# Kernel tuning notes

Hardware: AMD Instinct MI355X
Metric: run time of the kernel (lower is better)

The kernel has to match this reference:

```python
import jax, jax.numpy as jnp
import numpy as np


def _lstm_scan(x_seq, W, U, b):
    # x_seq: [T, in_dim]; Keras gate order i, f, g(c), o; sigmoid/tanh activations.
    units = W.shape[1] // 4
    xz = x_seq @ W + b  # [T, 4*units], precompute input contribution

    def step(carry, xz_t):
        h, c = carry
        z = xz_t + h @ U
        i, f, g, o = jnp.split(z, 4)
        i = jax.nn.sigmoid(i)
        f = jax.nn.sigmoid(f)
        g = jnp.tanh(g)
        o = jax.nn.sigmoid(o)
        c_new = f * c + i * g
        h_new = o * jnp.tanh(c_new)
        return (h_new, c_new), h_new

    h0 = jnp.zeros((units,), dtype=x_seq.dtype)
    c0 = jnp.zeros((units,), dtype=x_seq.dtype)
    (_, _), hs = jax.lax.scan(step, (h0, c0), xz)
    return hs  # [T, units]


def setup_inputs() -> dict:
    key = jax.random.key(0)
    ks = jax.random.split(key, 6)
    var_num, g_dim, d, vocab = 256, 1024, 512, 32000
    s = lambda fi, fo: (2.0 / (fi + fo)) ** 0.5
    return {
        "context": jax.random.normal(ks[0], (var_num, g_dim), jnp.float32),
        "Wm": jax.random.normal(ks[1], (g_dim, d), jnp.float32) * s(g_dim, d),
        "bm": jnp.zeros((d,), jnp.float32),
        "W": jax.random.normal(ks[2], (d, 4 * d), jnp.float32) * s(d, 4 * d),
        "U": jax.random.normal(ks[3], (d, 4 * d), jnp.float32) * s(d, 4 * d),
        "b": jnp.zeros((4 * d,), jnp.float32),
        "Wl": jax.random.normal(ks[4], (d, vocab), jnp.float32) * s(d, vocab),
        "bl": jnp.zeros((vocab,), jnp.float32),
        "max_subtoken_len": 8,
    }


def reference(context, Wm, bm, W, U, b, Wl, bl, max_subtoken_len):
    # Dense merge of func/graph embedding (cat_func_g_emb branch)
    merged = context @ Wm + bm  # [var_num, d]
    var_num = merged.shape[0]
    # Original loop feeds the SAME [1, var_num, d] sequence through the LSTM
    # max_subtoken_len times, carrying (h, c) across iterations => one long
    # scan over the tiled sequence of length S * var_num.
    x_seq = jnp.tile(merged, (max_subtoken_len, 1))  # [S*var_num, d]
    hs = _lstm_scan(x_seq, W, U, b)  # [S*var_num, units]
    hs = hs.reshape(max_subtoken_len, var_num, -1)  # [S, var_num, units]
    logits = jnp.einsum("svd,dk->svk", hs, Wl) + bl  # [S, var_num, vocab]
    return jnp.transpose(logits, (1, 0, 2))  # [var_num, S, vocab]
```

## Files before the change

kernel.cpp:

```cpp
#include <hip/hip_runtime.h>
#include <stdint.h>

#define D 512
#define T 2048
#define VOCAB 32000
#define NWG 16

typedef __attribute__((ext_vector_type(8))) short short8;
typedef __attribute__((ext_vector_type(4))) float f32x4;
typedef __attribute__((ext_vector_type(8))) unsigned short u16x8;
typedef __attribute__((ext_vector_type(2))) __fp16 f16x2;

__device__ __forceinline__ float fast_rcp(float x) { return __builtin_amdgcn_rcpf(x); }
__device__ __forceinline__ float sigm(float x) { return fast_rcp(1.0f + __expf(-x)); }
__device__ __forceinline__ float tanh_fast(float x) {
  float e = __expf(2.0f * x);
  return 1.0f - 2.0f * fast_rcp(e + 1.0f);
}
__device__ __forceinline__ unsigned short f2bf(float f) {
  unsigned u = __float_as_uint(f);
  unsigned r = u + 0x7fffu + ((u >> 16) & 1u);
  return (unsigned short)(r >> 16);
}
__device__ __forceinline__ uint64_t AL(const uint64_t* p) {
  return __hip_atomic_load(p, __ATOMIC_RELAXED, __HIP_MEMORY_SCOPE_AGENT);
}
union U32H2 { unsigned u; f16x2 h; };

__global__ __launch_bounds__(512) void prep_kernel(
    const float* __restrict__ ctx, const float* __restrict__ Wm,
    const float* __restrict__ bm, const float* __restrict__ W,
    const float* __restrict__ b, float* __restrict__ xz)
{
  __shared__ float ctx_s[4][1024];
  __shared__ float mg_s[4][512];
  const int tid = threadIdx.x;
  const int r0 = blockIdx.x * 4;

  for (int i = tid; i < 1024; i += 512) {
    int rr = i >> 8, c4 = (i & 255) * 4;
    *(float4*)&ctx_s[rr][c4] = *(const float4*)&ctx[(size_t)(r0 + rr) * 1024 + c4];
  }
  __syncthreads();
  {
    const int rr = tid >> 7, cg = (tid & 127) * 4;
    float a0 = bm[cg], a1 = bm[cg + 1], a2 = bm[cg + 2], a3 = bm[cg + 3];
    for (int k = 0; k < 1024; k += 4) {
      float4 cv = *(float4*)&ctx_s[rr][k];
      #pragma unroll
      for (int kk = 0; kk < 4; kk++) {
        float cc = (kk == 0) ? cv.x : (kk == 1) ? cv.y : (kk == 2) ? cv.z : cv.w;
        float4 wv = *(const float4*)&Wm[(size_t)(k + kk) * 512 + cg];
        a0 += cc * wv.x; a1 += cc * wv.y; a2 += cc * wv.z; a3 += cc * wv.w;
      }
    }
    *(float4*)&mg_s[rr][cg] = make_float4(a0, a1, a2, a3);
  }
  __syncthreads();
  {
    const int rr = tid >> 7, cg = (tid & 127) * 16;
    float acc[16];
    #pragma unroll
    for (int c = 0; c < 16; c++) acc[c] = b[cg + c];
    for (int k = 0; k < 512; k += 4) {
      float4 mv = *(float4*)&mg_s[rr][k];
      #pragma unroll
      for (int kk = 0; kk < 4; kk++) {
        float cc = (kk == 0) ? mv.x : (kk == 1) ? mv.y : (kk == 2) ? mv.z : mv.w;
        #pragma unroll
        for (int c4 = 0; c4 < 4; c4++) {
          float4 wv = *(const float4*)&W[(size_t)(k + kk) * 2048 + cg + c4 * 4];
          acc[c4 * 4 + 0] += cc * wv.x; acc[c4 * 4 + 1] += cc * wv.y;
          acc[c4 * 4 + 2] += cc * wv.z; acc[c4 * 4 + 3] += cc * wv.w;
        }
      }
    }
    #pragma unroll
    for (int c4 = 0; c4 < 4; c4++)
      *(float4*)&xz[(size_t)(r0 + rr) * 2048 + cg + c4 * 4] =
          make_float4(acc[c4 * 4], acc[c4 * 4 + 1], acc[c4 * 4 + 2], acc[c4 * 4 + 3]);
  }
}

__global__ __launch_bounds__(256) void wl_convert_kernel(
    const float* __restrict__ Wl, unsigned short* __restrict__ Wlt)
{
  const int c = blockIdx.x * 256 + threadIdx.x;
  for (int k8 = 0; k8 < 64; k8++) {
    u16x8 v;
    #pragma unroll
    for (int e = 0; e < 8; e++)
      v[e] = f2bf(Wl[(size_t)(k8 * 8 + e) * VOCAB + c]);
    *(u16x8*)&Wlt[(size_t)c * 512 + k8 * 8] = v;
  }
}

__global__ __launch_bounds__(256) void uconv2_kernel(
    const float* __restrict__ U, unsigned* __restrict__ Upr)
{
  const int blk = blockIdx.x;
  const int wg = blk >> 4, cb = blk & 15;
  const int rb = threadIdx.x & 31, ep = threadIdx.x >> 5;
  const int u0 = wg * 32 + cb * 2;
  const int r = rb + 64 * ep;
  unsigned outv[8];
  #pragma unroll
  for (int g = 0; g < 4; g++) {
    float2 lo = *(const float2*)&U[(size_t)r * 2048 + g * 512 + u0];
    float2 hi = *(const float2*)&U[(size_t)(r + 32) * 2048 + g * 512 + u0];
    U32H2 w0; w0.h[0] = (__fp16)lo.x; w0.h[1] = (__fp16)hi.x;
    U32H2 w1; w1.h[0] = (__fp16)lo.y; w1.h[1] = (__fp16)hi.y;
    outv[g * 2] = w0.u; outv[g * 2 + 1] = w1.u;
  }
  unsigned* dst = Upr + ((size_t)(wg * 512 + cb * 32 + rb)) * 64 + ep * 8;
  *(uint4*)dst = make_uint4(outv[0], outv[1], outv[2], outv[3]);
  *(uint4*)(dst + 4) = make_uint4(outv[4], outv[5], outv[6], outv[7]);
}

__global__
__attribute__((amdgpu_flat_work_group_size(512, 512)))
__attribute__((amdgpu_waves_per_eu(2, 2)))
void lstm_kernel(
    const float* __restrict__ xz, const unsigned* __restrict__ Upr,
    uint64_t* __restrict__ hb, unsigned short* __restrict__ hs)
{
  __shared__ float h_lds[2][512];
  const int tid = threadIdx.x;
  const int wg = blockIdx.x;
  const int rb = tid & 31;
  const int lane = tid & 63;
  const int cb = tid >> 5;
  const int u0 = wg * 32 + cb * 2;
  const bool gl = (rb < 2);
  const bool mypoll = (tid < 128) && ((tid >> 3) != wg);

  const unsigned* ubase = Upr + ((size_t)(wg * 512 + tid)) * 64;
  uint4 uv[16];
  #pragma unroll
  for (int i = 0; i < 16; i++) {
    const unsigned* ap = ubase + i * 4;
    asm volatile("global_load_dwordx4 %0, %1, off" : "=v"(uv[i]) : "v"(ap));
  }
  asm volatile("s_waitcnt vmcnt(0)" ::: "memory");
  unsigned u2[8][8];
  #pragma unroll
  for (int ep = 0; ep < 8; ep++) {
    uint4 a = uv[ep * 2], b4 = uv[ep * 2 + 1];
    u2[ep][0] = a.x; u2[ep][1] = a.y; u2[ep][2] = a.z; u2[ep][3] = a.w;
    u2[ep][4] = b4.x; u2[ep][5] = b4.y; u2[ep][6] = b4.z; u2[ep][7] = b4.w;
  }

  h_lds[0][tid] = 0.0f;
  float creg = 0.0f;
  const int b0 = rb & 1, b1 = (rb >> 1) & 1, b2v = (rb >> 2) & 1;

  for (int t = 0; t < T; t++) {
    #pragma unroll
    for (int ep = 0; ep < 8; ep++) {
      #pragma unroll
      for (int c = 0; c < 8; c++) asm volatile("" : "+v"(u2[ep][c]));
    }
    float xv0, xv1, xv2, xv3;
    if (gl) {
      const float* xp = &xz[(size_t)(t & 255) * 2048 + u0 + rb];
      xv0 = xp[0]; xv1 = xp[512]; xv2 = xp[1024]; xv3 = xp[1536];
    }
    const int par = t & 1;
    if (mypoll) {
      uint64_t* hw = hb + ((size_t)par << 9) + tid * 4;
      const unsigned tt = (unsigned)t;
      for (;;) {
        uint64_t w0 = AL(hw), w1 = AL(hw + 1), w2 = AL(hw + 2), w3 = AL(hw + 3);
        if (((unsigned)(w0 >> 32) == tt) & ((unsigned)(w1 >> 32) == tt) &
            ((unsigned)(w2 >> 32) == tt) & ((unsigned)(w3 >> 32) == tt)) {
          h_lds[par][tid * 4 + 0] = __uint_as_float((unsigned)w0);
          h_lds[par][tid * 4 + 1] = __uint_as_float((unsigned)w1);
          h_lds[par][tid * 4 + 2] = __uint_as_float((unsigned)w2);
          h_lds[par][tid * 4 + 3] = __uint_as_float((unsigned)w3);
          break;
        }
      }
    }
    __syncthreads();

    float zp[8];
    #pragma unroll
    for (int c = 0; c < 8; c++) zp[c] = 0.0f;
    #pragma unroll
    for (int ep = 0; ep < 8; ep++) {
      float hlo = h_lds[par][rb + 64 * ep];
      float hhi = h_lds[par][rb + 64 * ep + 32];
      f16x2 h2 = __builtin_amdgcn_cvt_pkrtz(hlo, hhi);
      #pragma unroll
      for (int c = 0; c < 8; c++) {
        U32H2 w; w.u = u2[ep][c];
        zp[c] = __builtin_amdgcn_fdot2(h2, w.h, zp[c], false);
      }
    }
    float q[4];
    #pragma unroll
    for (int j = 0; j < 4; j++) {
      float send = b0 ? zp[2 * j] : zp[2 * j + 1];
      float recv = __shfl_xor(send, 1, 64);
      q[j] = (b0 ? zp[2 * j + 1] : zp[2 * j]) + recv;
    }
    float r2[2];
    #pragma unroll
    for (int j = 0; j < 2; j++) {
      float send = b1 ? q[2 * j] : q[2 * j + 1];
      float recv = __shfl_xor(send, 2, 64);
      r2[j] = (b1 ? q[2 * j + 1] : q[2 * j]) + recv;
    }
    float z;
    {
      float send = b2v ? r2[0] : r2[1];
      float recv = __shfl_xor(send, 4, 64);
      z = (b2v ? r2[1] : r2[0]) + recv;
    }
    z += __shfl_xor(z, 8, 64);
    z += __shfl_xor(z, 16, 64);
    float zf = __shfl(z, (lane & 32) + 2 + b0, 64);
    float zg = __shfl(z, (lane & 32) + 4 + b0, 64);
    float zo = __shfl(z, (lane & 32) + 6 + b0, 64);

    if (gl) {
      float ig = sigm(z + xv0);
      float fg = sigm(zf + xv1);
      float gg = tanh_fast(zg + xv2);
      float og = sigm(zo + xv3);
      creg = fg * creg + ig * gg;
      float h = og * tanh_fast(creg);
      uint64_t pk = ((uint64_t)(unsigned)(t + 1) << 32) | (uint64_t)__float_as_uint(h);
      __hip_atomic_store(&hb[((size_t)((t + 1) & 1) << 9) + u0 + rb], pk,
                         __ATOMIC_RELAXED, __HIP_MEMORY_SCOPE_AGENT);
      h_lds[(t + 1) & 1][u0 + rb] = h;
      hs[(size_t)t * 512 + u0 + rb] = f2bf(h);
    }
  }
}

__global__ __launch_bounds__(512) void logits_kernel(
    const unsigned short* __restrict__ hs, const unsigned short* __restrict__ Wlt,
    const float* __restrict__ bl, float* __restrict__ out)
{
  __shared__ unsigned short As[128][40];
  __shared__ unsigned short Bs[256][40];
  const int tid = threadIdx.x;
  const int bx = blockIdx.x, by = blockIdx.y;
  const int lane = tid & 63, w = tid >> 6;
  const int wr = w >> 2, wc = w & 3;

  f32x4 acc[4][4];
  #pragma unroll
  for (int i = 0; i < 4; i++) {
    #pragma unroll
    for (int j = 0; j < 4; j++) acc[i][j] = (f32x4){0.0f, 0.0f, 0.0f, 0.0f};
  }

  for (int kk = 0; kk < 512; kk += 32) {
    {
      int r = tid >> 2, c8 = (tid & 3) * 8;
      *(uint4*)&As[r][c8] = *(const uint4*)&hs[(size_t)(by * 128 + r) * 512 + kk + c8];
    }
    #pragma unroll
    for (int i = 0; i < 2; i++) {
      int chunk = tid * 2 + i;
      int r = chunk >> 2, c8 = (chunk & 3) * 8;
      *(uint4*)&Bs[r][c8] = *(const uint4*)&Wlt[(size_t)(bx * 256 + r) * 512 + kk + c8];
    }
    __syncthreads();
    short8 af[4], bf[4];
    #pragma unroll
    for (int fr = 0; fr < 4; fr++)
      af[fr] = *(const short8*)&As[wr * 64 + fr * 16 + (lane & 15)][(lane >> 4) * 8];
    #pragma unroll
    for (int fc = 0; fc < 4; fc++)
      bf[fc] = *(const short8*)&Bs[wc * 64 + fc * 16 + (lane & 15)][(lane >> 4) * 8];
    #pragma unroll
    for (int fr = 0; fr < 4; fr++) {
      #pragma unroll
      for (int fc = 0; fc < 4; fc++)
        acc[fr][fc] = __builtin_amdgcn_mfma_f32_16x16x32_bf16(af[fr], bf[fc], acc[fr][fc], 0, 0, 0);
    }
    __syncthreads();
  }

  #pragma unroll
  for (int fc = 0; fc < 4; fc++) {
    int col = bx * 256 + wc * 64 + fc * 16 + (lane & 15);
    float blv = bl[col];
    #pragma unroll
    for (int fr = 0; fr < 4; fr++) {
      int row0 = by * 128 + wr * 64 + fr * 16 + (lane >> 4) * 4;
      #pragma unroll
      for (int j = 0; j < 4; j++) {
        int row = row0 + j;
        int orow = (row & 255) * 8 + (row >> 8);
        out[(size_t)orow * VOCAB + col] = acc[fr][fc][j] + blv;
      }
    }
  }
}

extern "C" void kernel_launch(void* const* d_in, const int* in_sizes, int n_in,
                              void* d_out, int out_size, void* d_ws, size_t ws_size,
                              hipStream_t stream)
{
  const float* ctx = (const float*)d_in[0];
  const float* Wm  = (const float*)d_in[1];
  const float* bm  = (const float*)d_in[2];
  const float* W   = (const float*)d_in[3];
  const float* U   = (const float*)d_in[4];
  const float* b   = (const float*)d_in[5];
  const float* Wl  = (const float*)d_in[6];
  const float* bl  = (const float*)d_in[7];
  float* out = (float*)d_out;

  char* ws = (char*)d_ws;
  uint64_t* hb        = (uint64_t*)ws;
  float* xz           = (float*)(ws + 65536);
  unsigned short* hs  = (unsigned short*)(ws + 65536 + (1 << 21));
  unsigned* Upr       = (unsigned*)(ws + 65536 + (2 << 21));
  unsigned short* Wlt = (unsigned short*)(ws + 65536 + (3 << 21));

  hipMemsetAsync(hb, 0, 8192, stream);
  prep_kernel<<<dim3(64), dim3(512), 0, stream>>>(ctx, Wm, bm, W, b, xz);
  uconv2_kernel<<<dim3(256), dim3(256), 0, stream>>>(U, Upr);
  wl_convert_kernel<<<dim3(125), dim3(256), 0, stream>>>(Wl, Wlt);

  void* args[] = { (void*)&xz, (void*)&Upr, (void*)&hb, (void*)&hs };
  hipLaunchCooperativeKernel((void*)lstm_kernel, dim3(NWG), dim3(512), args, 0, stream);

  logits_kernel<<<dim3(125, 16), dim3(512), 0, stream>>>(hs, Wlt, bl, out);
}
```

Measured before the change: 4.759 ms.

## Split LSTM workgroup into compute and polling waves with 256-thread reduction

The recurrent kernel now gives the first 256 threads the matvec, with each thread holding twice as many fp16 U weights in registers and reducing over 16 lanes instead of 32. The other 256 threads only poll the global h buffer for the next step and write it into LDS. The next step's xz values are prefetched right after the gate math, so their latency overlaps the poll. This aims to shorten the shuffle reduction and hide synchronization latency, at the cost of more registers per compute thread and a slower U repacking kernel launched with only 16 blocks.

Measured after the change: 4.834 ms. Within noise of the previous version (+1.6%).

```diff
diff --git a/kernel.cpp b/kernel.cpp
--- a/kernel.cpp
+++ b/kernel.cpp
@@ -95,26 +95,28 @@
   }
 }
 
-__global__ __launch_bounds__(256) void uconv2_kernel(
+__global__ __launch_bounds__(256) void uconv3_kernel(
     const float* __restrict__ U, unsigned* __restrict__ Upr)
 {
-  const int blk = blockIdx.x;
-  const int wg = blk >> 4, cb = blk & 15;
-  const int rb = threadIdx.x & 31, ep = threadIdx.x >> 5;
-  const int u0 = wg * 32 + cb * 2;
-  const int r = rb + 64 * ep;
-  unsigned outv[8];
-  #pragma unroll
-  for (int g = 0; g < 4; g++) {
-    float2 lo = *(const float2*)&U[(size_t)r * 2048 + g * 512 + u0];
-    float2 hi = *(const float2*)&U[(size_t)(r + 32) * 2048 + g * 512 + u0];
-    U32H2 w0; w0.h[0] = (__fp16)lo.x; w0.h[1] = (__fp16)hi.x;
-    U32H2 w1; w1.h[0] = (__fp16)lo.y; w1.h[1] = (__fp16)hi.y;
-    outv[g * 2] = w0.u; outv[g * 2 + 1] = w1.u;
-  }
-  unsigned* dst = Upr + ((size_t)(wg * 512 + cb * 32 + rb)) * 64 + ep * 8;
-  *(uint4*)dst = make_uint4(outv[0], outv[1], outv[2], outv[3]);
-  *(uint4*)(dst + 4) = make_uint4(outv[4], outv[5], outv[6], outv[7]);
+  const int wg = blockIdx.x;
+  const int tid = threadIdx.x;
+  const int g = tid >> 4, l = tid & 15;
+  const int u0 = wg * 32 + g * 2;
+  unsigned* dst = Upr + ((size_t)(wg * 256 + tid)) * 128;
+  for (int ep = 0; ep < 16; ep++) {
+    const int r = l + 16 * ep;
+    unsigned outv[8];
+    #pragma unroll
+    for (int c = 0; c < 8; c++) {
+      const int col = (c >> 1) * 512 + u0 + (c & 1);
+      U32H2 w;
+      w.h[0] = (__fp16)U[(size_t)r * 2048 + col];
+      w.h[1] = (__fp16)U[(size_t)(r + 256) * 2048 + col];
+      outv[c] = w.u;
+    }
+    *(uint4*)(dst + ep * 8)     = make_uint4(outv[0], outv[1], outv[2], outv[3]);
+    *(uint4*)(dst + ep * 8 + 4) = make_uint4(outv[4], outv[5], outv[6], outv[7]);
+  }
 }
 
 __global__
@@ -127,115 +129,118 @@
   __shared__ float h_lds[2][512];
   const int tid = threadIdx.x;
   const int wg = blockIdx.x;
-  const int rb = tid & 31;
+  const bool is_comp = (tid < 256);
+
+  h_lds[0][tid] = 0.0f;
+
+  const int g = tid >> 4, l = tid & 15;
   const int lane = tid & 63;
-  const int cb = tid >> 5;
-  const int u0 = wg * 32 + cb * 2;
-  const bool gl = (rb < 2);
-  const bool mypoll = (tid < 128) && ((tid >> 3) != wg);
-
-  const unsigned* ubase = Upr + ((size_t)(wg * 512 + tid)) * 64;
-  uint4 uv[16];
-  #pragma unroll
-  for (int i = 0; i < 16; i++) {
-    const unsigned* ap = ubase + i * 4;
-    asm volatile("global_load_dwordx4 %0, %1, off" : "=v"(uv[i]) : "v"(ap));
-  }
-  asm volatile("s_waitcnt vmcnt(0)" ::: "memory");
-  unsigned u2[8][8];
-  #pragma unroll
-  for (int ep = 0; ep < 8; ep++) {
-    uint4 a = uv[ep * 2], b4 = uv[ep * 2 + 1];
-    u2[ep][0] = a.x; u2[ep][1] = a.y; u2[ep][2] = a.z; u2[ep][3] = a.w;
-    u2[ep][4] = b4.x; u2[ep][5] = b4.y; u2[ep][6] = b4.z; u2[ep][7] = b4.w;
-  }
-
-  h_lds[0][tid] = 0.0f;
+  const int u0 = wg * 32 + g * 2;
+  const bool gl = is_comp && (l < 2);
+  const int b0 = l & 1, b1 = (l >> 1) & 1, b2v = (l >> 2) & 1;
+
+  unsigned u2[16][8];
+  float xv0 = 0.f, xv1 = 0.f, xv2 = 0.f, xv3 = 0.f;
+  if (is_comp) {
+    const unsigned* ubase = Upr + ((size_t)(wg * 256 + tid)) * 128;
+    uint4 uv[32];
+    #pragma unroll
+    for (int i = 0; i < 16; i++) {
+      const unsigned* ap = ubase + i * 8;
+      asm volatile("global_load_dwordx4 %0, %1, off"
+                   : "=v"(uv[i * 2]) : "v"(ap));
+      asm volatile("global_load_dwordx4 %0, %1, off offset:16"
+                   : "=v"(uv[i * 2 + 1]) : "v"(ap));
+    }
+    asm volatile("s_waitcnt vmcnt(0)" ::: "memory");
+    #pragma unroll
+    for (int ep = 0; ep < 16; ep++) {
+      uint4 a = uv[ep * 2], b4 = uv[ep * 2 + 1];
+      u2[ep][0] = a.x; u2[ep][1] = a.y; u2[ep][2] = a.z; u2[ep][3] = a.w;
+      u2[ep][4] = b4.x; u2[ep][5] = b4.y; u2[ep][6] = b4.z; u2[ep][7] = b4.w;
+    }
+    if (gl) {
+      const float* xp = &xz[(size_t)0 * 2048 + u0 + l];
+      xv0 = xp[0]; xv1 = xp[512]; xv2 = xp[1024]; xv3 = xp[1536];
+    }
+  }
   float creg = 0.0f;
-  const int b0 = rb & 1, b1 = (rb >> 1) & 1, b2v = (rb >> 2) & 1;
+  __syncthreads();
 
   for (int t = 0; t < T; t++) {
-    #pragma unroll
-    for (int ep = 0; ep < 8; ep++) {
-      #pragma unroll
-      for (int c = 0; c < 8; c++) asm volatile("" : "+v"(u2[ep][c]));
-    }
-    float xv0, xv1, xv2, xv3;
-    if (gl) {
-      const float* xp = &xz[(size_t)(t & 255) * 2048 + u0 + rb];
-      xv0 = xp[0]; xv1 = xp[512]; xv2 = xp[1024]; xv3 = xp[1536];
-    }
-    const int par = t & 1;
-    if (mypoll) {
-      uint64_t* hw = hb + ((size_t)par << 9) + tid * 4;
-      const unsigned tt = (unsigned)t;
+    if (is_comp) {
+      #pragma unroll
+      for (int ep = 0; ep < 16; ep++) {
+        #pragma unroll
+        for (int c = 0; c < 8; c++) asm volatile("" : "+v"(u2[ep][c]));
+      }
+      const int par = t & 1;
+      float zp[8];
+      #pragma unroll
+      for (int c = 0; c < 8; c++) zp[c] = 0.0f;
+      #pragma unroll
+      for (int ep = 0; ep < 16; ep++) {
+        float hlo = h_lds[par][l + 16 * ep];
+        float hhi = h_lds[par][l + 16 * ep + 256];
+        f16x2 h2 = __builtin_amdgcn_cvt_pkrtz(hlo, hhi);
+        #pragma unroll
+        for (int c = 0; c < 8; c++) {
+          U32H2 w; w.u = u2[ep][c];
+          zp[c] = __builtin_amdgcn_fdot2(h2, w.h, zp[c], false);
+        }
+      }
+      float q[4];
+      #pragma unroll
+      for (int j = 0; j < 4; j++) {
+        float send = b0 ? zp[2 * j] : zp[2 * j + 1];
+        float recv = __shfl_xor(send, 1, 64);
+        q[j] = (b0 ? zp[2 * j + 1] : zp[2 * j]) + recv;
+      }
+      float r2[2];
+      #pragma unroll
+      for (int j = 0; j < 2; j++) {
+        float send = b1 ? q[2 * j] : q[2 * j + 1];
+        float recv = __shfl_xor(send, 2, 64);
+        r2[j] = (b1 ? q[2 * j + 1] : q[2 * j]) + recv;
+      }
+      float z;
+      {
+        float send = b2v ? r2[0] : r2[1];
+        float recv = __shfl_xor(send, 4, 64);
+        z = (b2v ? r2[1] : r2[0]) + recv;
+      }
+      z += __shfl_xor(z, 8, 64);
+      float zf = __shfl(z, (lane & 48) + 2 + b0, 64);
+      float zg = __shfl(z, (lane & 48) + 4 + b0, 64);
+      float zo = __shfl(z, (lane & 48) + 6 + b0, 64);
+
+      if (gl) {
+        float ig = sigm(z + xv0);
+        float fg = sigm(zf + xv1);
+        float gg = tanh_fast(zg + xv2);
+        float og = sigm(zo + xv3);
+        creg = fg * creg + ig * gg;
+        float h = og * tanh_fast(creg);
+        uint64_t pk = ((uint64_t)(unsigned)(t + 1) << 32) | (uint64_t)__float_as_uint(h);
+        __hip_atomic_store(&hb[((size_t)((t + 1) & 1) << 9) + u0 + l], pk,
+                           __ATOMIC_RELAXED, __HIP_MEMORY_SCOPE_AGENT);
+        hs[(size_t)t * 512 + u0 + l] = f2bf(h);
+        const float* xp = &xz[(size_t)((t + 1) & 255) * 2048 + u0 + l];
+        xv0 = xp[0]; xv1 = xp[512]; xv2 = xp[1024]; xv3 = xp[1536];
+      }
+    } else {
+      const int pt = tid - 256;
+      uint64_t* hw = hb + ((size_t)((t + 1) & 1) << 9) + pt * 2;
+      const unsigned tt = (unsigned)(t + 1);
+      uint64_t w0, w1;
       for (;;) {
-        uint64_t w0 = AL(hw), w1 = AL(hw + 1), w2 = AL(hw + 2), w3 = AL(hw + 3);
-        if (((unsigned)(w0 >> 32) == tt) & ((unsigned)(w1 >> 32) == tt) &
-            ((unsigned)(w2 >> 32) == tt) & ((unsigned)(w3 >> 32) == tt)) {
-          h_lds[par][tid * 4 + 0] = __uint_as_float((unsigned)w0);
-          h_lds[par][tid * 4 + 1] = __uint_as_float((unsigned)w1);
-          h_lds[par][tid * 4 + 2] = __uint_as_float((unsigned)w2);
-          h_lds[par][tid * 4 + 3] = __uint_as_float((unsigned)w3);
-          break;
-        }
-      }
+        w0 = AL(hw); w1 = AL(hw + 1);
+        if (((unsigned)(w0 >> 32) == tt) & ((unsigned)(w1 >> 32) == tt)) break;
+      }
+      h_lds[(t + 1) & 1][pt * 2]     = __uint_as_float((unsigned)w0);
+      h_lds[(t + 1) & 1][pt * 2 + 1] = __uint_as_float((unsigned)w1);
     }
     __syncthreads();
-
-    float zp[8];
-    #pragma unroll
-    for (int c = 0; c < 8; c++) zp[c] = 0.0f;
-    #pragma unroll
-    for (int ep = 0; ep < 8; ep++) {
-      float hlo = h_lds[par][rb + 64 * ep];
-      float hhi = h_lds[par][rb + 64 * ep + 32];
-      f16x2 h2 = __builtin_amdgcn_cvt_pkrtz(hlo, hhi);
-      #pragma unroll
-      for (int c = 0; c < 8; c++) {
-        U32H2 w; w.u = u2[ep][c];
-        zp[c] = __builtin_amdgcn_fdot2(h2, w.h, zp[c], false);
-      }
-    }
-    float q[4];
-    #pragma unroll
-    for (int j = 0; j < 4; j++) {
-      float send = b0 ? zp[2 * j] : zp[2 * j + 1];
-      float recv = __shfl_xor(send, 1, 64);
-      q[j] = (b0 ? zp[2 * j + 1] : zp[2 * j]) + recv;
-    }
-    float r2[2];
-    #pragma unroll
-    for (int j = 0; j < 2; j++) {
-      float send = b1 ? q[2 * j] : q[2 * j + 1];
-      float recv = __shfl_xor(send, 2, 64);
-      r2[j] = (b1 ? q[2 * j + 1] : q[2 * j]) + recv;
-    }
-    float z;
-    {
-      float send = b2v ? r2[0] : r2[1];
-      float recv = __shfl_xor(send, 4, 64);
-      z = (b2v ? r2[1] : r2[0]) + recv;
-    }
-    z += __shfl_xor(z, 8, 64);
-    z += __shfl_xor(z, 16, 64);
-    float zf = __shfl(z, (lane & 32) + 2 + b0, 64);
-    float zg = __shfl(z, (lane & 32) + 4 + b0, 64);
-    float zo = __shfl(z, (lane & 32) + 6 + b0, 64);
-
-    if (gl) {
-      float ig = sigm(z + xv0);
-      float fg = sigm(zf + xv1);
-      float gg = tanh_fast(zg + xv2);
-      float og = sigm(zo + xv3);
-      creg = fg * creg + ig * gg;
-      float h = og * tanh_fast(creg);
-      uint64_t pk = ((uint64_t)(unsigned)(t + 1) << 32) | (uint64_t)__float_as_uint(h);
-      __hip_atomic_store(&hb[((size_t)((t + 1) & 1) << 9) + u0 + rb], pk,
-                         __ATOMIC_RELAXED, __HIP_MEMORY_SCOPE_AGENT);
-      h_lds[(t + 1) & 1][u0 + rb] = h;
-      hs[(size_t)t * 512 + u0 + rb] = f2bf(h);
-    }
   }
 }
 
@@ -325,7 +330,7 @@
 
   hipMemsetAsync(hb, 0, 8192, stream);
   prep_kernel<<<dim3(64), dim3(512), 0, stream>>>(ctx, Wm, bm, W, b, xz);
-  uconv2_kernel<<<dim3(256), dim3(256), 0, stream>>>(U, Upr);
+  uconv3_kernel<<<dim3(16), dim3(256), 0, stream>>>(U, Upr);
   wl_convert_kernel<<<dim3(125), dim3(256), 0, stream>>>(Wl, Wlt);
 
   void* args[] = { (void*)&xz, (void*)&Upr, (void*)&hb, (void*)&hs };
```
